# Performance work log

Measured on AMD Instinct MI355X. Metric: run time of the kernel, lower is better.

The kernel has to match this reference:

```python
import jax, jax.numpy as jnp
import numpy as np

N, D, F, C = 50000, 16, 128, 40  # nodes, fixed neighbor count, feat dim (hidden/2), classes


def _w(k, shape, fan_in):
    return jax.random.normal(k, shape, jnp.float32) / np.float32(np.sqrt(fan_in))


def setup_inputs() -> dict:
    key = jax.random.key(0)
    ks = jax.random.split(key, 8)
    z = lambda *s: jnp.zeros(s, jnp.float32)
    inp = {
        "x": jax.random.normal(ks[0], (N, F), jnp.float32),
        "edge_src": jax.random.randint(ks[1], (N, D), 0, N),  # dst is implicitly arange(N), sorted
        "W1": _w(ks[2], (F, F), F), "b1": z(F),
        "W2": _w(ks[3], (3 * F, F), F), "b2": z(3 * F),
        "W3": _w(ks[4], (F, 3 * F), 3 * F), "b3": z(F),
    }
    for i, (kb, oc) in (("1", (ks[5], F)), ("2", (ks[6], C))):
        pass  # placeholder (loop built below)
    for i, kb, oc in (("1", ks[5], F), ("2", ks[6], C)):
        kk = jax.random.split(kb, 5)
        inp["Wp" + i] = _w(kk[0], (F, F), F); inp["bp" + i] = z(F)
        inp["Wih" + i] = _w(kk[1], (4 * F, F), F)
        inp["Whh" + i] = _w(kk[2], (4 * F, F), F)
        inp["bih" + i] = z(4 * F); inp["bhh" + i] = z(4 * F)
        inp["Wl" + i] = _w(kk[3], (oc, F), F); inp["bl" + i] = z(oc)
        inp["Wr" + i] = _w(kk[4], (oc, F), F)
    return inp


def lstm_last(seq, Wih, Whh, bih, bhh):
    """seq: [N, T, F] -> final hidden state [N, H] (torch LSTM gate order i,f,g,o)."""
    Hh = Whh.shape[1]
    b = bih + bhh

    def step(carry, xt):
        h, c = carry
        g = xt @ Wih.T + h @ Whh.T + b
        i, f, gg, o = jnp.split(g, 4, axis=-1)
        c = jax.nn.sigmoid(f) * c + jax.nn.sigmoid(i) * jnp.tanh(gg)
        h = jax.nn.sigmoid(o) * jnp.tanh(c)
        return (h, c), None

    h0 = jnp.zeros((seq.shape[0], Hh), seq.dtype)
    (h, _), _ = jax.lax.scan(step, (h0, h0), jnp.swapaxes(seq, 0, 1))
    return h


def sage_conv_lstm(x, edge_src, Wp, bp, Wih, Whh, bih, bhh, Wl, bl, Wr):
    """PyG SAGEConv(aggr='lstm', project=True) with fixed per-node degree D."""
    xp = jax.nn.relu(x @ Wp.T + bp)           # project source features
    msgs = xp[edge_src]                        # [N, D, F] neighbor gather (sorted by dst)
    aggr = lstm_last(msgs, Wih, Whh, bih, bhh)  # LSTM over each neighborhood
    return aggr @ Wl.T + bl + x @ Wr.T         # lin_l(aggr) + lin_r(root)


def reference(x, edge_src, W1, b1, W2, b2, W3, b3,
              Wp1, bp1, Wih1, Whh1, bih1, bhh1, Wl1, bl1, Wr1,
              Wp2, bp2, Wih2, Whh2, bih2, bhh2, Wl2, bl2, Wr2):
    # Dead MLP branch: original forward computes it then overwrites h with conv1(x, ...)
    h = jax.nn.relu(x @ W1.T + b1)
    h = jax.nn.relu(h @ W2.T + b2)
    h = jax.nn.relu(h @ W3.T + b3)
    del h
    h = jax.nn.relu(sage_conv_lstm(x, edge_src, Wp1, bp1, Wih1, Whh1, bih1, bhh1, Wl1, bl1, Wr1))
    return sage_conv_lstm(h, edge_src, Wp2, bp2, Wih2, Whh2, bih2, bhh2, Wl2, bl2, Wr2)
```

## Files before the change

### kernel.cpp

```cpp
#include <hip/hip_runtime.h>
#include <hip/hip_bf16.h>


typedef __hip_bfloat16 bf16;
typedef __attribute__((ext_vector_type(8))) short short8;
typedef __attribute__((ext_vector_type(4))) short short4v;
typedef __attribute__((ext_vector_type(4))) float floatx4;
typedef __attribute__((ext_vector_type(4))) float float4v;

#define LOG2E 1.4426950408889634f
#define TWOL  2.8853900817779268f

__device__ __forceinline__ float bf2f(bf16 v) { return __bfloat162float(v); }
__device__ __forceinline__ bf16  f2bf(float v) { return __float2bfloat16(v); }
__device__ __forceinline__ float bfs2f(short s) {
    union { float f; unsigned u; } v; v.u = ((unsigned)(unsigned short)s) << 16; return v.f;
}
__device__ __forceinline__ short f2bfs(float v) {
    bf16 b = __float2bfloat16(v); return *(short*)&b;
}

__device__ __forceinline__ float ex2(float x) {
#if __has_builtin(__builtin_amdgcn_exp2f)
    return __builtin_amdgcn_exp2f(x);
#else
    return exp2f(x);
#endif
}

__device__ __forceinline__ float cell(float i_, float f_, float g_, float o_, float& c) {
    float ei = ex2(-i_), ef = ex2(-f_), eg = ex2(g_), eo = ex2(-o_);
    float A = (1.f + ei) * (eg + 1.f);
    float B = 1.f + ef;
    float cn = fmaf(c, A, fmaf(eg, TWOL, -TWOL) * B) * __builtin_amdgcn_rcpf(A * B);
    c = cn;
    float ec = ex2(cn);
    return (ec - 1.f) * __builtin_amdgcn_rcpf((ec + 1.f) * (1.f + eo));
}

__device__ __forceinline__ int ydecode(int p) {
    int pw = (p >> 6) & 7, pq = (p >> 4) & 3, pg = (p >> 2) & 3, pr = p & 3;
    return pg * 128 + pw * 16 + pq * 4 + pr;
}

__device__ __forceinline__ void dma1(const bf16* gp, void* lp) {
    __builtin_amdgcn_global_load_lds(
        (const __attribute__((address_space(1))) void*)gp,
        (__attribute__((address_space(3))) void*)lp, 16, 0, 0);
}

__device__ __forceinline__ void dma2(const bf16* gp, void* lp0, void* lp1) {
    dma1(gp, lp0);
    dma1(gp + 32, lp1);
}

struct Cvt { const void* src; const void* src2; bf16* dst; int n; int mode; };
struct CvtAll { Cvt t[17]; };

__global__ void convert_inputs(CvtAll ca, int* __restrict__ flag) {
    __shared__ int sflag;
    {
        const unsigned short* xb = (const unsigned short*)ca.t[0].src;
        int cnt = 0;
        for (int i = threadIdx.x; i < 1024; i += blockDim.x) {
            int e = (xb[i] >> 7) & 0xFF;
            cnt += (e >= 0xC8);
        }
        if (threadIdx.x == 0) sflag = 0;
        __syncthreads();
        if (cnt) atomicAdd(&sflag, cnt);
        __syncthreads();
    }
    const bool isf32 = (sflag >= 16);
    if (blockIdx.x == 0 && threadIdx.x == 0) *flag = isf32 ? 1 : 0;

    const int stride = gridDim.x * blockDim.x;
    const int tid0 = blockIdx.x * blockDim.x + threadIdx.x;
#pragma unroll 1
    for (int k = 0; k < 17; k++) {
        const int n = ca.t[k].n, mode = ca.t[k].mode;
        if (mode == 3) {
            const float* a32 = (const float*)ca.t[k].src;
            const float* b32 = (const float*)ca.t[k].src2;
            const short* a16 = (const short*)ca.t[k].src;
            const short* b16 = (const short*)ca.t[k].src2;
            float* df = (float*)ca.t[k].dst;
            for (int i = tid0; i < n; i += stride) {
                int yd = ydecode(i);
                float va = isf32 ? a32[yd] : bfs2f(a16[yd]);
                float vb = isf32 ? b32[yd] : bfs2f(b16[yd]);
                float m = ((((unsigned)i >> 2) & 3) == 2) ? TWOL : LOG2E;
                df[i] = (va + vb) * m;
            }
            continue;
        }
        const int n8 = n >> 3;
        bf16* d = ca.t[k].dst;
        for (int i = tid0; i < n8; i += stride) {
            int si = i;
            float m = 1.f;
            bool scaled = false;
            if (mode == 1) {
                m = ((((unsigned)i >> 11) & 3) == 2) ? TWOL : LOG2E; scaled = true;
            } else if (mode == 2) {
                int row = i >> 4;
                si = ydecode(row) * 16 + (i & 15);
                m = ((((unsigned)row >> 2) & 3) == 2) ? TWOL : LOG2E; scaled = true;
            }
            short8 ov;
            if (isf32) {
                const float4v* sp = (const float4v*)ca.t[k].src;
                float4v a = sp[2 * si], b = sp[2 * si + 1];
#pragma unroll
                for (int j = 0; j < 4; j++) {
                    ov[j]     = f2bfs(a[j] * m);
                    ov[4 + j] = f2bfs(b[j] * m);
                }
            } else {
                short8 sv = ((const short8*)ca.t[k].src)[si];
                if (scaled) {
#pragma unroll
                    for (int j = 0; j < 8; j++) ov[j] = f2bfs(bfs2f(sv[j]) * m);
                } else ov = sv;
            }
            ((short8*)d)[i] = ov;
        }
        if (mode == 0)
            for (int i = (n8 << 3) + tid0; i < n; i += stride) {
                float v = isf32 ? ((const float*)ca.t[k].src)[i]
                                : bfs2f(((const short*)ca.t[k].src)[i]);
                d[i] = f2bf(v);
            }
    }
}

__global__ __launch_bounds__(256, 2) void fused_xp_y(
    const bf16* __restrict__ X, const bf16* __restrict__ Wp, const bf16* __restrict__ bp,
    const bf16* __restrict__ Wihp, const float* __restrict__ bsum,
    bf16* __restrict__ Yout, int N)
{
    __shared__ bf16 T[64][136];
    const int tid = threadIdx.x;
    const int w = tid >> 6, l = tid & 63, q = l >> 4, lid = l & 15;
    const int rowbase = blockIdx.x * 64;

    int arow = rowbase + w * 16 + lid;
    if (arow >= N) arow = N - 1;

    floatx4 acc[8];
    short8 bfrag[8][4];
    float bvv[8];

#pragma unroll
    for (int ct = 0; ct < 8; ct++) acc[ct] = (floatx4)(0.f);
#pragma unroll
    for (int ct = 0; ct < 8; ct++) {
        int j = lid * 8 + ct;
        bvv[ct] = bf2f(bp[j]);
#pragma unroll
        for (int kt = 0; kt < 4; kt++)
            bfrag[ct][kt] = *(const short8*)(Wp + (size_t)j * 128 + kt * 32 + q * 8);
    }
#pragma unroll
    for (int kt = 0; kt < 4; kt++) {
        short8 af = *(const short8*)(X + (size_t)arow * 128 + kt * 32 + q * 8);
#pragma unroll
        for (int ct = 0; ct < 8; ct++)
            acc[ct] = __builtin_amdgcn_mfma_f32_16x16x32_bf16(af, bfrag[ct][kt], acc[ct], 0, 0, 0);
    }
#pragma unroll
    for (int r = 0; r < 4; r++) {
        short8 ov;
#pragma unroll
        for (int ct = 0; ct < 8; ct++)
            ov[ct] = f2bfs(fmaxf(acc[ct][r] + bvv[ct], 0.f));
        *(short8*)&T[w * 16 + q * 4 + r][lid * 8] = ov;
    }
    __syncthreads();

#pragma unroll
    for (int ct = 0; ct < 8; ct++) {
        int pos = w * 128 + lid * 8 + ct;
        bvv[ct] = bsum[pos];
#pragma unroll
        for (int kt = 0; kt < 4; kt++)
            bfrag[ct][kt] = *(const short8*)(Wihp + (size_t)pos * 128 + kt * 32 + q * 8);
    }
#pragma unroll 1
    for (int rt = 0; rt < 4; rt++) {
#pragma unroll
        for (int ct = 0; ct < 8; ct++) acc[ct] = (floatx4)(0.f);
#pragma unroll
        for (int kt = 0; kt < 4; kt++) {
            short8 af = *(const short8*)&T[rt * 16 + lid][kt * 32 + q * 8];
#pragma unroll
            for (int ct = 0; ct < 8; ct++)
                acc[ct] = __builtin_amdgcn_mfma_f32_16x16x32_bf16(af, bfrag[ct][kt], acc[ct], 0, 0, 0);
        }
#pragma unroll
        for (int r = 0; r < 4; r++) {
            int row = rowbase + rt * 16 + q * 4 + r;
            if (row < N) {
                short8 ov;
#pragma unroll
                for (int ct = 0; ct < 8; ct++)
                    ov[ct] = f2bfs(acc[ct][r] + bvv[ct]);
                *(short8*)(Yout + (size_t)row * 512 + w * 128 + lid * 8) = ov;
            }
        }
    }
}

__global__ __launch_bounds__(256, 2) void fused_lin_xp_y(
    const bf16* __restrict__ aggr, const bf16* __restrict__ Wl, const bf16* __restrict__ bl,
    const bf16* __restrict__ X, const bf16* __restrict__ Wr,
    bf16* __restrict__ h1out,
    const bf16* __restrict__ Wp2, const bf16* __restrict__ bp2,
    const bf16* __restrict__ Wihp2, const float* __restrict__ bsum2,
    bf16* __restrict__ Yout, int N)
{
    __shared__ bf16 T1[64][136];
    __shared__ bf16 T2[64][136];
    const int tid = threadIdx.x;
    const int w = tid >> 6, l = tid & 63, q = l >> 4, lid = l & 15;
    const int rowbase = blockIdx.x * 64;

    int arow = rowbase + w * 16 + lid;
    if (arow >= N) arow = N - 1;

    floatx4 acc[8];
    short8 bfrag[8][4];
    float bvv[8];

#pragma unroll
    for (int ct = 0; ct < 8; ct++) acc[ct] = (floatx4)(0.f);
#pragma unroll
    for (int ct = 0; ct < 8; ct++) {
        int j = lid * 8 + ct;
        bvv[ct] = bf2f(bl[j]);
#pragma unroll
        for (int kt = 0; kt < 4; kt++)
            bfrag[ct][kt] = *(const short8*)(Wl + (size_t)j * 128 + kt * 32 + q * 8);
    }
#pragma unroll
    for (int kt = 0; kt < 4; kt++) {
        short8 af = *(const short8*)(aggr + (size_t)arow * 128 + kt * 32 + q * 8);
#pragma unroll
        for (int ct = 0; ct < 8; ct++)
            acc[ct] = __builtin_amdgcn_mfma_f32_16x16x32_bf16(af, bfrag[ct][kt], acc[ct], 0, 0, 0);
    }
#pragma unroll
    for (int ct = 0; ct < 8; ct++) {
        int j = lid * 8 + ct;
#pragma unroll
        for (int kt = 0; kt < 4; kt++)
            bfrag[ct][kt] = *(const short8*)(Wr + (size_t)j * 128 + kt * 32 + q * 8);
    }
#pragma unroll
    for (int kt = 0; kt < 4; kt++) {
        short8 af = *(const short8*)(X + (size_t)arow * 128 + kt * 32 + q * 8);
#pragma unroll
        for (int ct = 0; ct < 8; ct++)
            acc[ct] = __builtin_amdgcn_mfma_f32_16x16x32_bf16(af, bfrag[ct][kt], acc[ct], 0, 0, 0);
    }
#pragma unroll
    for (int r = 0; r < 4; r++) {
        short8 ov;
#pragma unroll
        for (int ct = 0; ct < 8; ct++)
            ov[ct] = f2bfs(fmaxf(acc[ct][r] + bvv[ct], 0.f));
        int rl = w * 16 + q * 4 + r;
        *(short8*)&T1[rl][lid * 8] = ov;
        int row = rowbase + rl;
        if (row < N) *(short8*)(h1out + (size_t)row * 128 + lid * 8) = ov;
    }
    __syncthreads();

#pragma unroll
    for (int ct = 0; ct < 8; ct++) {
        int j = lid * 8 + ct;
        bvv[ct] = bf2f(bp2[j]);
#pragma unroll
        for (int kt = 0; kt < 4; kt++)
            bfrag[ct][kt] = *(const short8*)(Wp2 + (size_t)j * 128 + kt * 32 + q * 8);
    }
#pragma unroll
    for (int ct = 0; ct < 8; ct++) acc[ct] = (floatx4)(0.f);
#pragma unroll
    for (int kt = 0; kt < 4; kt++) {
        short8 af = *(const short8*)&T1[w * 16 + lid][kt * 32 + q * 8];
#pragma unroll
        for (int ct = 0; ct < 8; ct++)
            acc[ct] = __builtin_amdgcn_mfma_f32_16x16x32_bf16(af, bfrag[ct][kt], acc[ct], 0, 0, 0);
    }
#pragma unroll
    for (int r = 0; r < 4; r++) {
        short8 ov;
#pragma unroll
        for (int ct = 0; ct < 8; ct++)
            ov[ct] = f2bfs(fmaxf(acc[ct][r] + bvv[ct], 0.f));
        *(short8*)&T2[w * 16 + q * 4 + r][lid * 8] = ov;
    }
    __syncthreads();

#pragma unroll
    for (int ct = 0; ct < 8; ct++) {
        int pos = w * 128 + lid * 8 + ct;
        bvv[ct] = bsum2[pos];
#pragma unroll
        for (int kt = 0; kt < 4; kt++)
            bfrag[ct][kt] = *(const short8*)(Wihp2 + (size_t)pos * 128 + kt * 32 + q * 8);
    }
#pragma unroll 1
    for (int rt = 0; rt < 4; rt++) {
#pragma unroll
        for (int ct = 0; ct < 8; ct++) acc[ct] = (floatx4)(0.f);
#pragma unroll
        for (int kt = 0; kt < 4; kt++) {
            short8 af = *(const short8*)&T2[rt * 16 + lid][kt * 32 + q * 8];
#pragma unroll
            for (int ct = 0; ct < 8; ct++)
                acc[ct] = __builtin_amdgcn_mfma_f32_16x16x32_bf16(af, bfrag[ct][kt], acc[ct], 0, 0, 0);
        }
#pragma unroll
        for (int r = 0; r < 4; r++) {
            int row = rowbase + rt * 16 + q * 4 + r;
            if (row < N) {
                short8 ov;
#pragma unroll
                for (int ct = 0; ct < 8; ct++)
                    ov[ct] = f2bfs(acc[ct][r] + bvv[ct]);
                *(short8*)(Yout + (size_t)row * 512 + w * 128 + lid * 8) = ov;
            }
        }
    }
}

template <int EPI>
__global__ __launch_bounds__(512, 4) void lstm_aggr(
    const bf16* __restrict__ Y,
    const int* __restrict__ esrc,
    const bf16* __restrict__ Whh,
    bf16* __restrict__ aggr,
    int N,
    const bf16* __restrict__ Wl2, const bf16* __restrict__ bl2,
    const bf16* __restrict__ Wr2, const bf16* __restrict__ h1,
    void* __restrict__ outp, const int* __restrict__ oflag)
{
    __shared__ alignas(16) short stage[2][8][1024];
    __shared__ alignas(16) bf16 hb[2][16][136];
    __shared__ int srcl[16][16];

    const int tid = threadIdx.x;
    const int w = tid >> 6, l = tid & 63, q = l >> 4, lid = l & 15;
    const int nodebase = blockIdx.x * 16;

    if (tid < 256) {
        int node = tid >> 4, t = tid & 15;
        srcl[t][node] = esrc[(size_t)(nodebase + node) * 16 + t];
    }

    short8 wf[4][4];
#pragma unroll
    for (int g = 0; g < 4; g++) {
        int gc = g * 128 + 16 * w + lid;
#pragma unroll
        for (int kt = 0; kt < 4; kt++)
            wf[g][kt] = *(const short8*)(Whh + (size_t)gc * 128 + kt * 32 + q * 8);
    }

    float c[4];
#pragma unroll
    for (int r = 0; r < 4; r++) c[r] = 0.f;

    const int laneoff = w * 64 + q * 8;

    __syncthreads();

    {
        int s0 = srcl[0][lid];
        dma2(Y + (size_t)s0 * 512 + laneoff, &stage[0][w][0], &stage[0][w][512]);
        int s1 = srcl[1][lid];
        dma2(Y + (size_t)s1 * 512 + laneoff, &stage[1][w][0], &stage[1][w][512]);
    }

#pragma unroll 2
    for (int t = 0; t < 16; t++) {
        const int cb = t & 1;

        if (t == 15) asm volatile("s_waitcnt vmcnt(0)" ::: "memory");
        else         asm volatile("s_waitcnt vmcnt(2)" ::: "memory");

        if (EPI == 1 && t == 15 && w < 4) {
            const bf16* gp = h1 + (size_t)(nodebase + w * 4 + q) * 128 + lid * 8;
            dma1(gp, (char*)&stage[0][0][0] + (tid << 4 & ~1023 ? 0 : 0) + w * 1024);
        }

        int snext = (t < 14) ? srcl[t + 2][lid] : 0;

        floatx4 acc[4];
        {
            const short* wbuf = &stage[cb][w][0];
            short8 y0 = *(const short8*)&wbuf[q * 256 + lid * 8];
            short8 y1 = *(const short8*)&wbuf[q * 256 + 128 + lid * 8];
#pragma unroll
            for (int g = 0; g < 2; g++)
#pragma unroll
                for (int r = 0; r < 4; r++) {
                    acc[g][r]     = bfs2f(y0[g * 4 + r]);
                    acc[2 + g][r] = bfs2f(y1[g * 4 + r]);
                }
        }

        if (t) {
#pragma unroll
            for (int kt = 0; kt < 4; kt++) {
                short8 bh = *(const short8*)&hb[cb][lid][kt * 32 + q * 8];
#pragma unroll
                for (int g = 0; g < 4; g++)
                    acc[g] = __builtin_amdgcn_mfma_f32_16x16x32_bf16(wf[g][kt], bh, acc[g], 0, 0, 0);
            }
        }

        {
            short4v hv;
#pragma unroll
            for (int r = 0; r < 4; r++)
                hv[r] = f2bfs(cell(acc[0][r], acc[1][r], acc[2][r], acc[3][r], c[r]));
            if (t < 15) *(short4v*)&hb[cb ^ 1][lid][16 * w + 4 * q] = hv;
            else if (EPI == 0)
                *(short4v*)(aggr + (size_t)(nodebase + lid) * 128 + 16 * w + 4 * q) = hv;
            else
                *(short4v*)&hb[0][lid][16 * w + 4 * q] = hv;
        }

        if (t < 15) {
            asm volatile("s_waitcnt lgkmcnt(0)" ::: "memory");
            if (t < 14)
                dma2(Y + (size_t)snext * 512 + laneoff, &stage[cb][w][0], &stage[cb][w][512]);
            __builtin_amdgcn_s_barrier();
        }
    }

    if constexpr (EPI == 1) {
        asm volatile("s_waitcnt vmcnt(0)" ::: "memory");
        short8 blf[4], brf[4];
        int j = w * 16 + lid;
        int jc = j < 40 ? j : 39;
        if (w < 3) {
#pragma unroll
            for (int kt = 0; kt < 4; kt++) {
                blf[kt] = *(const short8*)(Wl2 + (size_t)jc * 128 + kt * 32 + q * 8);
                brf[kt] = *(const short8*)(Wr2 + (size_t)jc * 128 + kt * 32 + q * 8);
            }
        }
        asm volatile("s_waitcnt lgkmcnt(0)" ::: "memory");
        __builtin_amdgcn_s_barrier();
        if (w < 3) {
            const short* h1b = &stage[0][0][0];
            floatx4 o = (floatx4)(0.f);
#pragma unroll
            for (int kt = 0; kt < 4; kt++) {
                short8 ah = *(const short8*)&hb[0][lid][kt * 32 + q * 8];
                o = __builtin_amdgcn_mfma_f32_16x16x32_bf16(ah, blf[kt], o, 0, 0, 0);
            }
#pragma unroll
            for (int kt = 0; kt < 4; kt++) {
                short8 a1 = *(const short8*)&h1b[lid * 128 + kt * 32 + q * 8];
                o = __builtin_amdgcn_mfma_f32_16x16x32_bf16(a1, brf[kt], o, 0, 0, 0);
            }
            float bv = bf2f(bl2[jc]);
            bool of32 = (*oflag != 0);
            if (j < 40) {
#pragma unroll
                for (int r = 0; r < 4; r++) {
                    int node = nodebase + q * 4 + r;
                    float v = o[r] + bv;
                    size_t idx = (size_t)node * 40 + j;
                    if (of32) ((float*)outp)[idx] = v;
                    else      ((bf16*)outp)[idx]  = f2bf(v);
                }
            }
        }
    }
}

extern "C" void kernel_launch(void* const* d_in, const int* in_sizes, int n_in,
                              void* d_out, int out_size, void* d_ws, size_t ws_size,
                              hipStream_t stream)
{
    const int N = 50000;
    const int* es = (const int*)d_in[1];
    char* ws = (char*)d_ws;

    struct Ent { int di; int di2; int mode; };
    Ent ents[17] = {
        {0,  -1, 0},
        {8,  -1, 0}, {9,  -1, 0},
        {10, -1, 2}, {11, -1, 1},
        {12, 13, 3},
        {14, -1, 0}, {15, -1, 0}, {16, -1, 0},
        {17, -1, 0}, {18, -1, 0},
        {19, -1, 2}, {20, -1, 1},
        {21, 22, 3},
        {23, -1, 0}, {24, -1, 0}, {25, -1, 0},
    };
    bf16* conv[17];
    size_t off = 0;
    CvtAll ca;
    for (int k = 0; k < 17; k++) {
        conv[k] = (bf16*)ws + off;
        int n = in_sizes[ents[k].di];
        ca.t[k].src  = d_in[ents[k].di];
        ca.t[k].src2 = ents[k].di2 >= 0 ? d_in[ents[k].di2] : nullptr;
        ca.t[k].dst  = conv[k];
        ca.t[k].n    = n;
        ca.t[k].mode = ents[k].mode;
        size_t elems = (ents[k].mode == 3) ? (size_t)n * 2 : (size_t)n;
        off += (elems + 63) & ~(size_t)63;
    }
    int* flag  = (int*)(ws + ((size_t)15 << 20));
    bf16* aggr = (bf16*)(ws + ((size_t)16 << 20));
    bf16* Y    = (bf16*)(ws + ((size_t)30 << 20));
    bf16* h1   = (bf16*)(ws + ((size_t)84 << 20));

    const bf16 *xc   = conv[0];
    const bf16 *Wp1  = conv[1],  *bp1 = conv[2];
    const bf16 *Wihp1 = conv[3], *Whh1 = conv[4];
    const float *bsum1 = (const float*)conv[5];
    const bf16 *Wl1 = conv[6], *bl1 = conv[7], *Wr1 = conv[8];
    const bf16 *Wp2 = conv[9], *bp2 = conv[10];
    const bf16 *Wihp2 = conv[11], *Whh2 = conv[12];
    const float *bsum2 = (const float*)conv[13];
    const bf16 *Wl2 = conv[14], *bl2 = conv[15], *Wr2 = conv[16];

    dim3 blk(256);
    const int gx = (N + 63) / 64;
    const int gl = N / 16;

    convert_inputs<<<dim3(1024), blk, 0, stream>>>(ca, flag);

    fused_xp_y<<<dim3(gx), blk, 0, stream>>>(xc, Wp1, bp1, Wihp1, bsum1, Y, N);
    lstm_aggr<0><<<dim3(gl), dim3(512), 0, stream>>>(
        Y, es, Whh1, aggr, N, nullptr, nullptr, nullptr, nullptr, nullptr, nullptr);

    fused_lin_xp_y<<<dim3(gx), blk, 0, stream>>>(
        aggr, Wl1, bl1, xc, Wr1, h1, Wp2, bp2, Wihp2, bsum2, Y, N);

    lstm_aggr<1><<<dim3(gl), dim3(512), 0, stream>>>(
        Y, es, Whh2, aggr, N, Wl2, bl2, Wr2, h1, d_out, flag);
}
```

Before: 575.4 us.

## Fuse layer-1 output linear and layer-2 input projections into LSTM epilogue

Removes the standalone fused_lin_xp_y kernel and folds its work into the epilogue of the first LSTM aggregation kernel (new EPI==2 mode). After the final hidden state, that epilogue applies lin_l plus lin_r with ReLU to produce h1, then the layer-2 projection and the input-gate GEMM, and writes Y2 directly. The aggr round-trip through global memory and one kernel launch go away. Root features are staged into LDS with an XOR swizzle to reduce bank conflicts. The cost is a longer, serialized epilogue at 16 nodes per block, with weights reloaded from global memory per block and scalar, uncoalesced per-element stores of h1 and Y2.

Measured after the change: 575.6 us. Within noise of the previous version (+0.0%).

```diff
diff --git a/kernel.cpp b/kernel.cpp
--- a/kernel.cpp
+++ b/kernel.cpp
@@ -211,140 +211,18 @@
     }
 }
 
-__global__ __launch_bounds__(256, 2) void fused_lin_xp_y(
-    const bf16* __restrict__ aggr, const bf16* __restrict__ Wl, const bf16* __restrict__ bl,
-    const bf16* __restrict__ X, const bf16* __restrict__ Wr,
-    bf16* __restrict__ h1out,
-    const bf16* __restrict__ Wp2, const bf16* __restrict__ bp2,
-    const bf16* __restrict__ Wihp2, const float* __restrict__ bsum2,
-    bf16* __restrict__ Yout, int N)
-{
-    __shared__ bf16 T1[64][136];
-    __shared__ bf16 T2[64][136];
-    const int tid = threadIdx.x;
-    const int w = tid >> 6, l = tid & 63, q = l >> 4, lid = l & 15;
-    const int rowbase = blockIdx.x * 64;
-
-    int arow = rowbase + w * 16 + lid;
-    if (arow >= N) arow = N - 1;
-
-    floatx4 acc[8];
-    short8 bfrag[8][4];
-    float bvv[8];
-
-#pragma unroll
-    for (int ct = 0; ct < 8; ct++) acc[ct] = (floatx4)(0.f);
-#pragma unroll
-    for (int ct = 0; ct < 8; ct++) {
-        int j = lid * 8 + ct;
-        bvv[ct] = bf2f(bl[j]);
-#pragma unroll
-        for (int kt = 0; kt < 4; kt++)
-            bfrag[ct][kt] = *(const short8*)(Wl + (size_t)j * 128 + kt * 32 + q * 8);
-    }
-#pragma unroll
-    for (int kt = 0; kt < 4; kt++) {
-        short8 af = *(const short8*)(aggr + (size_t)arow * 128 + kt * 32 + q * 8);
-#pragma unroll
-        for (int ct = 0; ct < 8; ct++)
-            acc[ct] = __builtin_amdgcn_mfma_f32_16x16x32_bf16(af, bfrag[ct][kt], acc[ct], 0, 0, 0);
-    }
-#pragma unroll
-    for (int ct = 0; ct < 8; ct++) {
-        int j = lid * 8 + ct;
-#pragma unroll
-        for (int kt = 0; kt < 4; kt++)
-            bfrag[ct][kt] = *(const short8*)(Wr + (size_t)j * 128 + kt * 32 + q * 8);
-    }
-#pragma unroll
-    for (int kt = 0; kt < 4; kt++) {
-        short8 af = *(const short8*)(X + (size_t)arow * 128 + kt * 32 + q * 8);
-#pragma unroll
-        for (int ct = 0; ct < 8; ct++)
-            acc[ct] = __builtin_amdgcn_mfma_f32_16x16x32_bf16(af, bfrag[ct][kt], acc[ct], 0, 0, 0);
-    }
-#pragma unroll
-    for (int r = 0; r < 4; r++) {
-        short8 ov;
-#pragma unroll
-        for (int ct = 0; ct < 8; ct++)
-            ov[ct] = f2bfs(fmaxf(acc[ct][r] + bvv[ct], 0.f));
-        int rl = w * 16 + q * 4 + r;
-        *(short8*)&T1[rl][lid * 8] = ov;
-        int row = rowbase + rl;
-        if (row < N) *(short8*)(h1out + (size_t)row * 128 + lid * 8) = ov;
-    }
-    __syncthreads();
-
-#pragma unroll
-    for (int ct = 0; ct < 8; ct++) {
-        int j = lid * 8 + ct;
-        bvv[ct] = bf2f(bp2[j]);
-#pragma unroll
-        for (int kt = 0; kt < 4; kt++)
-            bfrag[ct][kt] = *(const short8*)(Wp2 + (size_t)j * 128 + kt * 32 + q * 8);
-    }
-#pragma unroll
-    for (int ct = 0; ct < 8; ct++) acc[ct] = (floatx4)(0.f);
-#pragma unroll
-    for (int kt = 0; kt < 4; kt++) {
-        short8 af = *(const short8*)&T1[w * 16 + lid][kt * 32 + q * 8];
-#pragma unroll
-        for (int ct = 0; ct < 8; ct++)
-            acc[ct] = __builtin_amdgcn_mfma_f32_16x16x32_bf16(af, bfrag[ct][kt], acc[ct], 0, 0, 0);
-    }
-#pragma unroll
-    for (int r = 0; r < 4; r++) {
-        short8 ov;
-#pragma unroll
-        for (int ct = 0; ct < 8; ct++)
-            ov[ct] = f2bfs(fmaxf(acc[ct][r] + bvv[ct], 0.f));
-        *(short8*)&T2[w * 16 + q * 4 + r][lid * 8] = ov;
-    }
-    __syncthreads();
-
-#pragma unroll
-    for (int ct = 0; ct < 8; ct++) {
-        int pos = w * 128 + lid * 8 + ct;
-        bvv[ct] = bsum2[pos];
-#pragma unroll
-        for (int kt = 0; kt < 4; kt++)
-            bfrag[ct][kt] = *(const short8*)(Wihp2 + (size_t)pos * 128 + kt * 32 + q * 8);
-    }
-#pragma unroll 1
-    for (int rt = 0; rt < 4; rt++) {
-#pragma unroll
-        for (int ct = 0; ct < 8; ct++) acc[ct] = (floatx4)(0.f);
-#pragma unroll
-        for (int kt = 0; kt < 4; kt++) {
-            short8 af = *(const short8*)&T2[rt * 16 + lid][kt * 32 + q * 8];
-#pragma unroll
-            for (int ct = 0; ct < 8; ct++)
-                acc[ct] = __builtin_amdgcn_mfma_f32_16x16x32_bf16(af, bfrag[ct][kt], acc[ct], 0, 0, 0);
-        }
-#pragma unroll
-        for (int r = 0; r < 4; r++) {
-            int row = rowbase + rt * 16 + q * 4 + r;
-            if (row < N) {
-                short8 ov;
-#pragma unroll
-                for (int ct = 0; ct < 8; ct++)
-                    ov[ct] = f2bfs(acc[ct][r] + bvv[ct]);
-                *(short8*)(Yout + (size_t)row * 512 + w * 128 + lid * 8) = ov;
-            }
-        }
-    }
-}
-
 template <int EPI>
 __global__ __launch_bounds__(512, 4) void lstm_aggr(
     const bf16* __restrict__ Y,
     const int* __restrict__ esrc,
     const bf16* __restrict__ Whh,
-    bf16* __restrict__ aggr,
     int N,
+    const bf16* __restrict__ X, const bf16* __restrict__ Wl, const bf16* __restrict__ bl,
+    const bf16* __restrict__ Wr, const bf16* __restrict__ Wp2, const bf16* __restrict__ bp2,
+    const bf16* __restrict__ Wihp2, const float* __restrict__ bsum2,
+    bf16* __restrict__ h1out, bf16* __restrict__ Y2out,
     const bf16* __restrict__ Wl2, const bf16* __restrict__ bl2,
-    const bf16* __restrict__ Wr2, const bf16* __restrict__ h1,
+    const bf16* __restrict__ Wr2, const bf16* __restrict__ h1in,
     void* __restrict__ outp, const int* __restrict__ oflag)
 {
     __shared__ alignas(16) short stage[2][8][1024];
@@ -391,9 +269,11 @@
         if (t == 15) asm volatile("s_waitcnt vmcnt(0)" ::: "memory");
         else         asm volatile("s_waitcnt vmcnt(2)" ::: "memory");
 
-        if (EPI == 1 && t == 15 && w < 4) {
-            const bf16* gp = h1 + (size_t)(nodebase + w * 4 + q) * 128 + lid * 8;
-            dma1(gp, (char*)&stage[0][0][0] + (tid << 4 & ~1023 ? 0 : 0) + w * 1024);
+        if (EPI && t == 15 && w < 4) {
+            int row = w * 4 + q;
+            const bf16* src = (EPI == 2) ? X : h1in;
+            const bf16* gp = src + (size_t)(nodebase + row) * 128 + (lid ^ (row & 7)) * 8;
+            dma1(gp, (char*)&stage[0][0][0] + w * 1024);
         }
 
         int snext = (t < 14) ? srcl[t + 2][lid] : 0;
@@ -428,10 +308,7 @@
             for (int r = 0; r < 4; r++)
                 hv[r] = f2bfs(cell(acc[0][r], acc[1][r], acc[2][r], acc[3][r], c[r]));
             if (t < 15) *(short4v*)&hb[cb ^ 1][lid][16 * w + 4 * q] = hv;
-            else if (EPI == 0)
-                *(short4v*)(aggr + (size_t)(nodebase + lid) * 128 + 16 * w + 4 * q) = hv;
-            else
-                *(short4v*)&hb[0][lid][16 * w + 4 * q] = hv;
+            else        *(short4v*)&hb[0][lid][16 * w + 4 * q] = hv;
         }
 
         if (t < 15) {
@@ -441,6 +318,8 @@
             __builtin_amdgcn_s_barrier();
         }
     }
+
+    const short* xs = &stage[0][0][0];
 
     if constexpr (EPI == 1) {
         asm volatile("s_waitcnt vmcnt(0)" ::: "memory");
@@ -457,7 +336,6 @@
         asm volatile("s_waitcnt lgkmcnt(0)" ::: "memory");
         __builtin_amdgcn_s_barrier();
         if (w < 3) {
-            const short* h1b = &stage[0][0][0];
             floatx4 o = (floatx4)(0.f);
 #pragma unroll
             for (int kt = 0; kt < 4; kt++) {
@@ -466,7 +344,7 @@
             }
 #pragma unroll
             for (int kt = 0; kt < 4; kt++) {
-                short8 a1 = *(const short8*)&h1b[lid * 128 + kt * 32 + q * 8];
+                short8 a1 = *(const short8*)&xs[lid * 128 + (((kt * 4 + q) ^ (lid & 7)) << 3)];
                 o = __builtin_amdgcn_mfma_f32_16x16x32_bf16(a1, brf[kt], o, 0, 0, 0);
             }
             float bv = bf2f(bl2[jc]);
@@ -481,6 +359,80 @@
                     else      ((bf16*)outp)[idx]  = f2bf(v);
                 }
             }
+        }
+    }
+
+    if constexpr (EPI == 2) {
+        const int j = w * 16 + lid;
+        short8 wlf[4], wrf[4];
+#pragma unroll
+        for (int kt = 0; kt < 4; kt++) {
+            wlf[kt] = *(const short8*)(Wl + (size_t)j * 128 + kt * 32 + q * 8);
+            wrf[kt] = *(const short8*)(Wr + (size_t)j * 128 + kt * 32 + q * 8);
+        }
+        float blv = bf2f(bl[j]);
+        asm volatile("s_waitcnt vmcnt(0)" ::: "memory");
+        asm volatile("s_waitcnt lgkmcnt(0)" ::: "memory");
+        __builtin_amdgcn_s_barrier();
+
+        floatx4 o = (floatx4)(0.f);
+#pragma unroll
+        for (int kt = 0; kt < 4; kt++) {
+            short8 ah = *(const short8*)&hb[0][lid][kt * 32 + q * 8];
+            o = __builtin_amdgcn_mfma_f32_16x16x32_bf16(ah, wlf[kt], o, 0, 0, 0);
+        }
+#pragma unroll
+        for (int kt = 0; kt < 4; kt++) {
+            short8 ax = *(const short8*)&xs[lid * 128 + (((kt * 4 + q) ^ (lid & 7)) << 3)];
+            o = __builtin_amdgcn_mfma_f32_16x16x32_bf16(ax, wrf[kt], o, 0, 0, 0);
+        }
+        short8 wpf[4];
+#pragma unroll
+        for (int kt = 0; kt < 4; kt++)
+            wpf[kt] = *(const short8*)(Wp2 + (size_t)j * 128 + kt * 32 + q * 8);
+        float bpv = bf2f(bp2[j]);
+#pragma unroll
+        for (int r = 0; r < 4; r++) {
+            short v = f2bfs(fmaxf(o[r] + blv, 0.f));
+            hb[1][q * 4 + r][j] = *(bf16*)&v;
+            h1out[(size_t)(nodebase + q * 4 + r) * 128 + j] = *(bf16*)&v;
+        }
+        asm volatile("s_waitcnt lgkmcnt(0)" ::: "memory");
+        __builtin_amdgcn_s_barrier();
+
+        floatx4 o2 = (floatx4)(0.f);
+#pragma unroll
+        for (int kt = 0; kt < 4; kt++) {
+            short8 a1 = *(const short8*)&hb[1][lid][kt * 32 + q * 8];
+            o2 = __builtin_amdgcn_mfma_f32_16x16x32_bf16(a1, wpf[kt], o2, 0, 0, 0);
+        }
+#pragma unroll
+        for (int r = 0; r < 4; r++) {
+            short v = f2bfs(fmaxf(o2[r] + bpv, 0.f));
+            hb[0][q * 4 + r][j] = *(bf16*)&v;
+        }
+        asm volatile("s_waitcnt lgkmcnt(0)" ::: "memory");
+        __builtin_amdgcn_s_barrier();
+
+        short8 axf[4];
+#pragma unroll
+        for (int kt = 0; kt < 4; kt++)
+            axf[kt] = *(const short8*)&hb[0][lid][kt * 32 + q * 8];
+#pragma unroll 1
+        for (int tt = 0; tt < 4; tt++) {
+            int pos = w * 64 + tt * 16 + lid;
+            short8 wf2[4];
+#pragma unroll
+            for (int kt = 0; kt < 4; kt++)
+                wf2[kt] = *(const short8*)(Wihp2 + (size_t)pos * 128 + kt * 32 + q * 8);
+            float bs = bsum2[pos];
+            floatx4 o3 = (floatx4)(0.f);
+#pragma unroll
+            for (int kt = 0; kt < 4; kt++)
+                o3 = __builtin_amdgcn_mfma_f32_16x16x32_bf16(axf[kt], wf2[kt], o3, 0, 0, 0);
+#pragma unroll
+            for (int r = 0; r < 4; r++)
+                Y2out[(size_t)(nodebase + q * 4 + r) * 512 + pos] = f2bf(o3[r] + bs);
         }
     }
 }
@@ -519,10 +471,10 @@
         size_t elems = (ents[k].mode == 3) ? (size_t)n * 2 : (size_t)n;
         off += (elems + 63) & ~(size_t)63;
     }
-    int* flag  = (int*)(ws + ((size_t)15 << 20));
-    bf16* aggr = (bf16*)(ws + ((size_t)16 << 20));
-    bf16* Y    = (bf16*)(ws + ((size_t)30 << 20));
-    bf16* h1   = (bf16*)(ws + ((size_t)84 << 20));
+    int* flag  = (int*)(ws + ((size_t)14 << 20));
+    bf16* Y1   = (bf16*)(ws + ((size_t)15 << 20));
+    bf16* h1   = (bf16*)(ws + ((size_t)67 << 20));
+    bf16* Y2   = (bf16*)(ws + ((size_t)80 << 20));
 
     const bf16 *xc   = conv[0];
     const bf16 *Wp1  = conv[1],  *bp1 = conv[2];
@@ -540,13 +492,16 @@
 
     convert_inputs<<<dim3(1024), blk, 0, stream>>>(ca, flag);
 
-    fused_xp_y<<<dim3(gx), blk, 0, stream>>>(xc, Wp1, bp1, Wihp1, bsum1, Y, N);
-    lstm_aggr<0><<<dim3(gl), dim3(512), 0, stream>>>(
-        Y, es, Whh1, aggr, N, nullptr, nullptr, nullptr, nullptr, nullptr, nullptr);
-
-    fused_lin_xp_y<<<dim3(gx), blk, 0, stream>>>(
-        aggr, Wl1, bl1, xc, Wr1, h1, Wp2, bp2, Wihp2, bsum2, Y, N);
+    fused_xp_y<<<dim3(gx), blk, 0, stream>>>(xc, Wp1, bp1, Wihp1, bsum1, Y1, N);
+
+    lstm_aggr<2><<<dim3(gl), dim3(512), 0, stream>>>(
+        Y1, es, Whh1, N,
+        xc, Wl1, bl1, Wr1, Wp2, bp2, Wihp2, bsum2, h1, Y2,
+        nullptr, nullptr, nullptr, nullptr, nullptr, nullptr);
 
     lstm_aggr<1><<<dim3(gl), dim3(512), 0, stream>>>(
-        Y, es, Whh2, aggr, N, Wl2, bl2, Wr2, h1, d_out, flag);
-}
+        Y2, es, Whh2, N,
+        nullptr, nullptr, nullptr, nullptr, nullptr, nullptr, nullptr, nullptr,
+        nullptr, nullptr,
+        Wl2, bl2, Wr2, h1, d_out, flag);
+}
```
